# Kernel optimization log

Measured on AMD Instinct MI355X. Metric: run time of the kernel, lower is better.

The kernel has to match this reference:

```python
import jax, jax.numpy as jnp
import numpy as np

B, N, M, C1, C2 = 4, 8192, 2048, 128, 256
H1, H2 = 256, 128  # mlp = [C2+C1, 256, 128]
EPS_DIST = 1e-8
EPS_BN = 1e-5
K = 3


def setup_inputs() -> dict:
    key = jax.random.key(0)
    ks = jax.random.split(key, 6)
    return {
        "unknown": jax.random.normal(ks[0], (B, N, 3), dtype=jnp.float32),
        "known": jax.random.normal(ks[1], (B, M, 3), dtype=jnp.float32),
        "unknow_feats": jax.random.normal(ks[2], (B, C1, N), dtype=jnp.float32),
        "known_feats": jax.random.normal(ks[3], (B, C2, M), dtype=jnp.float32),
        "W1": jax.random.normal(ks[4], (H1, C1 + C2), dtype=jnp.float32) * 0.05,
        "g1": jnp.ones((H1,), jnp.float32),
        "b1": jnp.zeros((H1,), jnp.float32),
        "W2": jax.random.normal(ks[5], (H2, H1), dtype=jnp.float32) * 0.05,
        "g2": jnp.ones((H2,), jnp.float32),
        "b2": jnp.zeros((H2,), jnp.float32),
    }


def _bn_relu(x, g, b):
    # training-mode BatchNorm over (batch, spatial) axes for (B, C, N) tensor
    mean = jnp.mean(x, axis=(0, 2), keepdims=True)
    var = jnp.var(x, axis=(0, 2), keepdims=True)
    y = (x - mean) * jax.lax.rsqrt(var + EPS_BN) * g[None, :, None] + b[None, :, None]
    return jax.nn.relu(y)


def reference(unknown, known, unknow_feats, known_feats, W1, g1, b1, W2, g2, b2):
    # 3-NN: squared euclidean distances (B, N, M) via expansion (avoids B,N,M,3 temp)
    d2 = (
        jnp.sum(unknown * unknown, axis=-1)[:, :, None]
        + jnp.sum(known * known, axis=-1)[:, None, :]
        - 2.0 * jnp.einsum("bnc,bmc->bnm", unknown, known)
    )
    neg_d, idx = jax.lax.top_k(-d2, K)  # smallest-K squared dists
    dist = -neg_d  # (B, N, K), squared distances (pytorch3d knn_points convention)
    recip = 1.0 / (dist + EPS_DIST)
    weight = recip / jnp.sum(recip, axis=2, keepdims=True)  # (B, N, K)

    kf = jnp.swapaxes(known_feats, 1, 2)  # (B, M, C2)
    grouped = jax.vmap(lambda f, i: f[i])(kf, idx)  # (B, N, K, C2)
    interp = jnp.einsum("bnkc,bnk->bcn", grouped, weight)  # (B, C2, N)

    x = jnp.concatenate([interp, unknow_feats], axis=1)  # (B, C2+C1, N)
    x = _bn_relu(jnp.einsum("oc,bcn->bon", W1, x), g1, b1)
    x = _bn_relu(jnp.einsum("oc,bcn->bon", W2, x), g2, b2)
    return x  # (B, H2, N)
```

## Files before the change

kernel.cpp:

```cpp
#include <hip/hip_runtime.h>
#include <hip/hip_bf16.h>
#include <cstdint>
#include <cstddef>

typedef unsigned short u16;
typedef __attribute__((ext_vector_type(8))) short bf16x8;
typedef __attribute__((ext_vector_type(4))) float f32x4;

constexpr int Bn = 4;
constexpr int Nq = 8192;
constexpr int Mk = 2048;
constexpr int C1c = 128;
constexpr int C2c = 256;
constexpr int H1c = 256;
constexpr int H2c = 128;

__device__ __forceinline__ float bf2f(u16 u) {
    union { uint32_t i; float f; } v;
    v.i = (uint32_t)u << 16;
    return v.f;
}
__device__ __forceinline__ u16 f2bf(float f) {
    const uint32_t x = __float_as_uint(f);
    return (u16)((x + 0x7FFFu + ((x >> 16) & 1u)) >> 16);
}
__device__ __forceinline__ uint32_t cvtpk(float lo, float hi) {
    uint32_t r;
    asm("v_cvt_pk_bf16_f32 %0, %1, %2" : "=v"(r) : "v"(lo), "v"(hi));
    return r;
}

__global__ __launch_bounds__(256) void knn_prep_kernel(
    const float* __restrict__ W1, const float* __restrict__ W2,
    u16* __restrict__ W1b, u16* __restrict__ W2b,
    const float* __restrict__ KF, u16* __restrict__ Ptb,
    const float* __restrict__ unknown, const float* __restrict__ known,
    int* __restrict__ idx_out, float* __restrict__ w_out)
{
    __shared__ __align__(16) char smem[32768];
    const int bid = blockIdx.x;
    const int t = threadIdx.x;

    if (bid < 1024) {
        float4* kp = (float4*)smem;
        const int b = bid >> 8;
        const int n0 = (bid & 255) * 32;

        const float* kb = known + (size_t)b * Mk * 3;
        for (int i = t; i < Mk; i += 256) {
            const float x = kb[i * 3 + 0], y = kb[i * 3 + 1], z = kb[i * 3 + 2];
            kp[i] = make_float4(x, y, z, fmaf(x, x, fmaf(y, y, z * z)));
        }
        __syncthreads();

        const int q = n0 + (t >> 3);
        const int s = t & 7;
        const float* u = unknown + ((size_t)b * Nq + q) * 3;
        const float ux = u[0], uy = u[1], uz = u[2];
        const float nux = -2.0f * ux, nuy = -2.0f * uy, nuz = -2.0f * uz;
        const float uu = fmaf(ux, ux, fmaf(uy, uy, uz * uz));

        float d0 = 1e30f, d1 = 1e30f, d2 = 1e30f;
        int i0 = 0, i1 = 0, i2 = 0;

        auto ins = [&](float d, int i) {
            const bool c0 = d < d0, c1 = d < d1, c2 = d < d2;
            const float nd0 = fminf(d0, d);
            const float nd1 = __builtin_amdgcn_fmed3f(d0, d, d1);
            const float nd2 = __builtin_amdgcn_fmed3f(d1, d, d2);
            i2 = c1 ? i1 : (c2 ? i : i2);
            i1 = c0 ? i0 : (c1 ? i : i1);
            i0 = c0 ? i : i0;
            d0 = nd0; d1 = nd1; d2 = nd2;
        };

        #pragma unroll 8
        for (int it = 0; it < Mk / 8; ++it) {
            const int m = it * 8 + s;
            const float4 p = kp[m];
            const float d = fmaf(nux, p.x, fmaf(nuy, p.y, fmaf(nuz, p.z, p.w)));
            ins(d, m);
        }
        #pragma unroll
        for (int off = 1; off <= 4; off <<= 1) {
            const float e0 = __shfl_xor(d0, off), e1 = __shfl_xor(d1, off), e2 = __shfl_xor(d2, off);
            const int j0 = __shfl_xor(i0, off), j1 = __shfl_xor(i1, off), j2 = __shfl_xor(i2, off);
            ins(e0, j0);
            ins(e1, j1);
            ins(e2, j2);
        }
        if (s == 0) {
            const float f0 = d0 + uu, f1 = d1 + uu, f2 = d2 + uu;
            const float r0 = 1.0f / (f0 + 1e-8f);
            const float r1 = 1.0f / (f1 + 1e-8f);
            const float r2 = 1.0f / (f2 + 1e-8f);
            const float inv = 1.0f / (r0 + r1 + r2);
            const size_t base = ((size_t)b * Nq + q) * 3;
            idx_out[base + 0] = i0;
            idx_out[base + 1] = i1;
            idx_out[base + 2] = i2;
            w_out[base + 0] = r0 * inv;
            w_out[base + 1] = r1 * inv;
            w_out[base + 2] = r2 * inv;
        }
    } else if (bid < 1152) {
        const int cb = bid - 1024;
        const float* X = (cb < 96) ? W1 : W2;
        u16* Y = (cb < 96) ? W1b : W2b;
        const int i = ((cb < 96) ? cb : (cb - 96)) * 256 + t;
        const float4 v = *(const float4*)&X[(size_t)i * 4];
        ushort4 o;
        o.x = f2bf(v.x); o.y = f2bf(v.y); o.z = f2bf(v.z); o.w = f2bf(v.w);
        *(ushort4*)&Y[(size_t)i * 4] = o;
    } else {
        u16* As = (u16*)smem;
        u16* Bs = (u16*)(smem + 5120);
        const int f = bid - 1152;
        const int b = f >> 7;
        const int rem = f & 127;
        const int m0 = (rem >> 2) * 64;
        const int h0 = (rem & 3) * 64;
        const float* KFb = KF + (size_t)b * C2c * Mk;
        const int l = t & 63, wv = t >> 6;
        const int wr = wv >> 1, wc = wv & 1;

        f32x4 acc[2][2];
        const f32x4 z = {0.0f, 0.0f, 0.0f, 0.0f};
        acc[0][0] = z; acc[0][1] = z; acc[1][0] = z; acc[1][1] = z;

        const int cA = t >> 3;
        const int mcA = (t & 7) * 8;
        const int hB = t >> 2;
        const int khB = (t & 3) * 8;

        for (int kt = 0; kt < 8; ++kt) {
            const int kc = kt * 32;
            {
                const float* src = &KFb[(size_t)(kc + cA) * Mk + m0 + mcA];
                const float4 v0 = *(const float4*)&src[0];
                const float4 v1 = *(const float4*)&src[4];
                As[(mcA + 0) * 40 + cA] = f2bf(v0.x);
                As[(mcA + 1) * 40 + cA] = f2bf(v0.y);
                As[(mcA + 2) * 40 + cA] = f2bf(v0.z);
                As[(mcA + 3) * 40 + cA] = f2bf(v0.w);
                As[(mcA + 4) * 40 + cA] = f2bf(v1.x);
                As[(mcA + 5) * 40 + cA] = f2bf(v1.y);
                As[(mcA + 6) * 40 + cA] = f2bf(v1.z);
                As[(mcA + 7) * 40 + cA] = f2bf(v1.w);
            }
            {
                const float* src = &W1[(size_t)(h0 + hB) * 384 + kc + khB];
                const float4 v0 = *(const float4*)&src[0];
                const float4 v1 = *(const float4*)&src[4];
                u16 o[8] = {f2bf(v0.x), f2bf(v0.y), f2bf(v0.z), f2bf(v0.w),
                            f2bf(v1.x), f2bf(v1.y), f2bf(v1.z), f2bf(v1.w)};
                *(uint4*)&Bs[hB * 40 + khB] = *(const uint4*)o;
            }
            __syncthreads();
            bf16x8 af[2], bf[2];
            #pragma unroll
            for (int ff = 0; ff < 2; ++ff) {
                af[ff] = *(const bf16x8*)&As[(wr * 32 + ff * 16 + (l & 15)) * 40 + (l >> 4) * 8];
                bf[ff] = *(const bf16x8*)&Bs[(wc * 32 + ff * 16 + (l & 15)) * 40 + (l >> 4) * 8];
            }
            #pragma unroll
            for (int i = 0; i < 2; ++i)
                #pragma unroll
                for (int j = 0; j < 2; ++j)
                    acc[i][j] = __builtin_amdgcn_mfma_f32_16x16x32_bf16(af[i], bf[j], acc[i][j], 0, 0, 0);
            __syncthreads();
        }

        u16* Pb = Ptb + (size_t)b * Mk * 256;
        const int cb = l & 15, rg = (l >> 4) * 4;
        #pragma unroll
        for (int i = 0; i < 2; ++i) {
            #pragma unroll
            for (int r = 0; r < 4; ++r) {
                const int row = m0 + wr * 32 + i * 16 + rg + r;
                #pragma unroll
                for (int j = 0; j < 2; ++j)
                    Pb[(size_t)row * 256 + h0 + wc * 32 + j * 16 + cb] = f2bf(acc[i][j][r]);
            }
        }
    }
}

__global__ __launch_bounds__(256) void mfma_gemm2(
    const float* __restrict__ UF,
    const u16* __restrict__ Bt,
    u16* __restrict__ Cout,
    const u16* __restrict__ Ptb,
    const int* __restrict__ idx, const float* __restrict__ wgt,
    float* __restrict__ partS, float* __restrict__ partQ)
{
    __shared__ __align__(16) char smem[16384];
    __shared__ float redS[4][128], redQ[4][128];
    u16* As = (u16*)smem;
    u16* Bs = (u16*)(smem + 8192);
    float (*Ytmp)[128] = (float(*)[128])smem;

    const int b = blockIdx.z;
    const int m0 = blockIdx.x * 128, n0 = blockIdx.y * 128;
    const int t = threadIdx.x;
    const int l = t & 63, wv = t >> 6;
    const int wr = wv >> 1, wc = wv & 1;

    const float* UFb = UF + (size_t)b * C1c * Nq;
    const int p = t & 15;
    const int qg = t >> 4;
    const int rB0 = t >> 2, rB1v = (t + 256) >> 2;
    const int koB = (t & 3) * 8;

    f32x4 acc[4][4];
    const f32x4 z = {0.0f, 0.0f, 0.0f, 0.0f};
    #pragma unroll
    for (int i = 0; i < 4; ++i)
        #pragma unroll
        for (int j = 0; j < 4; ++j) acc[i][j] = z;

    float4 va0, va1, vb0, vb1;
    {
        const float* r0 = &UFb[(size_t)(2 * p) * Nq + m0 + qg * 8];
        const float* r1 = r0 + Nq;
        va0 = *(const float4*)&r0[0];
        va1 = *(const float4*)&r0[4];
        vb0 = *(const float4*)&r1[0];
        vb1 = *(const float4*)&r1[4];
    }
    uint4 b0 = *(const uint4*)&Bt[(size_t)(n0 + rB0) * 384 + koB];
    uint4 b1 = *(const uint4*)&Bt[(size_t)(n0 + rB1v) * 384 + koB];

    for (int kt = 0; kt < C1c / 32; ++kt) {
        {
            const float* la = (const float*)&va0;
            const float* lb = (const float*)&va1;
            const float* ha = (const float*)&vb0;
            const float* hb = (const float*)&vb1;
            #pragma unroll
            for (int i = 0; i < 8; ++i) {
                const int row = qg * 8 + i;
                const float lo = (i < 4) ? la[i] : lb[i - 4];
                const float hi = (i < 4) ? ha[i] : hb[i - 4];
                const int byte = row * 64 + ((((p >> 2) ^ (row & 3)) << 4)) + (p & 3) * 4;
                *(uint32_t*)((char*)As + byte) = cvtpk(lo, hi);
            }
        }
        *(uint4*)&Bs[(size_t)rB0 * 32 + koB] = b0;
        *(uint4*)&Bs[(size_t)rB1v * 32 + koB] = b1;
        __syncthreads();
        if (kt + 1 < C1c / 32) {
            const int k0 = (kt + 1) * 32;
            const float* r0 = &UFb[(size_t)(k0 + 2 * p) * Nq + m0 + qg * 8];
            const float* r1 = r0 + Nq;
            va0 = *(const float4*)&r0[0];
            va1 = *(const float4*)&r0[4];
            vb0 = *(const float4*)&r1[0];
            vb1 = *(const float4*)&r1[4];
            b0 = *(const uint4*)&Bt[(size_t)(n0 + rB0) * 384 + k0 + koB];
            b1 = *(const uint4*)&Bt[(size_t)(n0 + rB1v) * 384 + k0 + koB];
        }
        bf16x8 af[4], bf[4];
        #pragma unroll
        for (int f = 0; f < 4; ++f) {
            const int row = wr * 64 + f * 16 + (l & 15);
            af[f] = *(const bf16x8*)((char*)As + row * 64 + ((((l >> 4) ^ (l & 3)) << 4)));
            bf[f] = *(const bf16x8*)&Bs[(wc * 64 + f * 16 + (l & 15)) * 32 + (l >> 4) * 8];
        }
        #pragma unroll
        for (int i = 0; i < 4; ++i)
            #pragma unroll
            for (int j = 0; j < 4; ++j)
                acc[i][j] = __builtin_amdgcn_mfma_f32_16x16x32_bf16(af[i], bf[j], acc[i][j], 0, 0, 0);
        __syncthreads();
    }

    const int cb = l & 15;
    const int rg = (l >> 4) * 4;
    const int colblk = t & 15;
    const int rowblk = t >> 4;
    float s8[8] = {0, 0, 0, 0, 0, 0, 0, 0}, q8[8] = {0, 0, 0, 0, 0, 0, 0, 0};
    const u16* Pb = Ptb + (size_t)b * Mk * 256;

    for (int q = 0; q < 4; ++q) {
        __syncthreads();
        if (wr == (q >> 1)) {
            #pragma unroll
            for (int ii = 0; ii < 2; ++ii) {
                const int i = (q & 1) * 2 + ii;
                #pragma unroll
                for (int r = 0; r < 4; ++r) {
                    const int Rq = ii * 16 + rg + r;
                    #pragma unroll
                    for (int j = 0; j < 4; ++j)
                        Ytmp[Rq][wc * 64 + j * 16 + cb] = acc[i][j][r];
                }
            }
        }
        __syncthreads();
        #pragma unroll
        for (int rr = 0; rr < 2; ++rr) {
            const int Rq = rowblk * 2 + rr;
            const int R = m0 + q * 32 + Rq;
            const size_t ib = ((size_t)b * Nq + R) * 3;
            const int j0 = idx[ib], j1 = idx[ib + 1], j2 = idx[ib + 2];
            const float w0 = wgt[ib], w1 = wgt[ib + 1], w2 = wgt[ib + 2];
            const int c8 = colblk * 8;
            const int Cc0 = n0 + c8;
            const float* yrow = &Ytmp[Rq][c8];
            const float4 y0 = *(const float4*)&yrow[0];
            const float4 y1v = *(const float4*)&yrow[4];
            const uint4 p0 = *(const uint4*)&Pb[(size_t)j0 * 256 + Cc0];
            const uint4 p1 = *(const uint4*)&Pb[(size_t)j1 * 256 + Cc0];
            const uint4 p2 = *(const uint4*)&Pb[(size_t)j2 * 256 + Cc0];
            const u16* pp0 = (const u16*)&p0;
            const u16* pp1 = (const u16*)&p1;
            const u16* pp2 = (const u16*)&p2;
            const float* ya = (const float*)&y0;
            const float* yb = (const float*)&y1v;
            float v[8];
            #pragma unroll
            for (int c = 0; c < 8; ++c) {
                const float a = (c < 4) ? ya[c] : yb[c - 4];
                const float vv = a + w0 * bf2f(pp0[c]) + w1 * bf2f(pp1[c]) + w2 * bf2f(pp2[c]);
                v[c] = vv;
                s8[c] += vv;
                q8[c] += vv * vv;
            }
            uint4 o;
            uint32_t* po = (uint32_t*)&o;
            po[0] = cvtpk(v[0], v[1]);
            po[1] = cvtpk(v[2], v[3]);
            po[2] = cvtpk(v[4], v[5]);
            po[3] = cvtpk(v[6], v[7]);
            *(uint4*)&Cout[(size_t)b * Nq * 256 + (size_t)R * 256 + Cc0] = o;
        }
    }

    #pragma unroll
    for (int c = 0; c < 8; ++c) {
        s8[c] += __shfl_xor(s8[c], 16);
        s8[c] += __shfl_xor(s8[c], 32);
        q8[c] += __shfl_xor(q8[c], 16);
        q8[c] += __shfl_xor(q8[c], 32);
    }
    if (l < 16) {
        #pragma unroll
        for (int c = 0; c < 8; ++c) {
            redS[wv][l * 8 + c] = s8[c];
            redQ[wv][l * 8 + c] = q8[c];
        }
    }
    __syncthreads();
    if (t < 128) {
        const float S = redS[0][t] + redS[1][t] + redS[2][t] + redS[3][t];
        const float Q = redQ[0][t] + redQ[1][t] + redQ[2][t] + redQ[3][t];
        const int pblk = blockIdx.z * gridDim.x + blockIdx.x;
        partS[(size_t)pblk * 256 + blockIdx.y * 128 + t] = S;
        partQ[(size_t)pblk * 256 + blockIdx.y * 128 + t] = Q;
    }
}

__global__ __launch_bounds__(256) void bn1_finalize_mb(
    const float* __restrict__ pS, const float* __restrict__ pQ,
    const float* __restrict__ g, const float* __restrict__ beta,
    float* __restrict__ scale, float* __restrict__ bias)
{
    __shared__ float rs[256], rq[256];
    const int cc = threadIdx.x & 15;
    const int sl = threadIdx.x >> 4;
    const int ch = blockIdx.x * 16 + cc;
    float s = 0.0f, q = 0.0f;
    for (int i = sl; i < 256; i += 16) {
        s += pS[(size_t)i * 256 + ch];
        q += pQ[(size_t)i * 256 + ch];
    }
    rs[threadIdx.x] = s;
    rq[threadIdx.x] = q;
    __syncthreads();
    if (sl == 0) {
        for (int k = 1; k < 16; ++k) {
            s += rs[k * 16 + cc];
            q += rq[k * 16 + cc];
        }
        const float cnt = (float)(Bn * Nq);
        const float mean = s / cnt;
        const float var = q / cnt - mean * mean;
        const float rv = rsqrtf(var + 1e-5f);
        const float sc = g[ch] * rv;
        scale[ch] = sc;
        bias[ch] = beta[ch] - mean * sc;
    }
}

__device__ __forceinline__ uint4 bnx(uint4 x, const float* scs, const float* bis, int k) {
    const u16* p = (const u16*)&x;
    const float4 s0 = *(const float4*)&scs[k];
    const float4 s1 = *(const float4*)&scs[k + 4];
    const float4 b0 = *(const float4*)&bis[k];
    const float4 b1 = *(const float4*)&bis[k + 4];
    const float* sa = (const float*)&s0;
    const float* sb = (const float*)&s1;
    const float* ba = (const float*)&b0;
    const float* bb = (const float*)&b1;
    uint4 o;
    uint32_t* po = (uint32_t*)&o;
    #pragma unroll
    for (int w2 = 0; w2 < 2; ++w2) {
        const float a0 = fmaxf(0.0f, fmaf(bf2f(p[2 * w2 + 0]), sa[2 * w2 + 0], ba[2 * w2 + 0]));
        const float a1 = fmaxf(0.0f, fmaf(bf2f(p[2 * w2 + 1]), sa[2 * w2 + 1], ba[2 * w2 + 1]));
        po[w2] = cvtpk(a0, a1);
    }
    #pragma unroll
    for (int w2 = 0; w2 < 2; ++w2) {
        const float a0 = fmaxf(0.0f, fmaf(bf2f(p[4 + 2 * w2 + 0]), sb[2 * w2 + 0], bb[2 * w2 + 0]));
        const float a1 = fmaxf(0.0f, fmaf(bf2f(p[4 + 2 * w2 + 1]), sb[2 * w2 + 1], bb[2 * w2 + 1]));
        po[2 + w2] = cvtpk(a0, a1);
    }
    return o;
}

__global__ __launch_bounds__(256) void mfma_gemm3(
    const u16* __restrict__ W2b,
    const u16* __restrict__ Y,
    u16* __restrict__ y2b,
    const float* __restrict__ bn_s, const float* __restrict__ bn_b,
    float* __restrict__ partS, float* __restrict__ partQ)
{
    __shared__ u16 As[2048];
    __shared__ u16 Bs[4096];
    __shared__ float scs[256], bis[256];
    __shared__ float sS[2][64], sQ[2][64];

    const int b = blockIdx.z;
    const int m0 = blockIdx.x * 64;
    const int n0 = blockIdx.y * 128;
    const int t = threadIdx.x;
    const int l = t & 63, wv = t >> 6;
    const int wr = wv >> 1, wc = wv & 1;

    scs[t] = bn_s[t];
    bis[t] = bn_b[t];

    const u16* Yb = Y + (size_t)b * Nq * 256;
    const int rA = t >> 2;
    const int rB1 = (t + 256) >> 2;
    const int ko = (t & 3) * 8;

    f32x4 acc[2][4];
    const f32x4 z = {0.0f, 0.0f, 0.0f, 0.0f};
    #pragma unroll
    for (int i = 0; i < 2; ++i)
        #pragma unroll
        for (int j = 0; j < 4; ++j) acc[i][j] = z;

    uint4 a0 = *(const uint4*)&W2b[(size_t)(m0 + rA) * 256 + ko];
    uint4 b0 = *(const uint4*)&Yb[(size_t)(n0 + rA) * 256 + ko];
    uint4 b1 = *(const uint4*)&Yb[(size_t)(n0 + rB1) * 256 + ko];
    __syncthreads();

    for (int kt = 0; kt < 8; ++kt) {
        const int k = kt * 32 + ko;
        *(uint4*)&As[t * 8] = a0;
        *(uint4*)&Bs[t * 8] = bnx(b0, scs, bis, k);
        *(uint4*)&Bs[(t + 256) * 8] = bnx(b1, scs, bis, k);
        __syncthreads();
        if (kt + 1 < 8) {
            const int k0 = (kt + 1) * 32;
            a0 = *(const uint4*)&W2b[(size_t)(m0 + rA) * 256 + k0 + ko];
            b0 = *(const uint4*)&Yb[(size_t)(n0 + rA) * 256 + k0 + ko];
            b1 = *(const uint4*)&Yb[(size_t)(n0 + rB1) * 256 + k0 + ko];
        }
        bf16x8 af[2], bf[4];
        #pragma unroll
        for (int f = 0; f < 2; ++f)
            af[f] = *(const bf16x8*)&As[(wr * 32 + f * 16 + (l & 15)) * 32 + (l >> 4) * 8];
        #pragma unroll
        for (int f = 0; f < 4; ++f)
            bf[f] = *(const bf16x8*)&Bs[(wc * 64 + f * 16 + (l & 15)) * 32 + (l >> 4) * 8];
        #pragma unroll
        for (int i = 0; i < 2; ++i)
            #pragma unroll
            for (int j = 0; j < 4; ++j)
                acc[i][j] = __builtin_amdgcn_mfma_f32_16x16x32_bf16(af[i], bf[j], acc[i][j], 0, 0, 0);
        __syncthreads();
    }

    const int cb = l & 15;
    const int rg = (l >> 4) * 4;
    u16* ob = y2b + (size_t)b * H2c * Nq;
    #pragma unroll
    for (int i = 0; i < 2; ++i) {
        #pragma unroll
        for (int r = 0; r < 4; ++r) {
            const int Rl = wr * 32 + i * 16 + rg + r;
            #pragma unroll
            for (int j = 0; j < 4; ++j) {
                const int Cc = n0 + wc * 64 + j * 16 + cb;
                ob[(size_t)(m0 + Rl) * Nq + Cc] = f2bf(acc[i][j][r]);
            }
            float s = acc[i][0][r] + acc[i][1][r] + acc[i][2][r] + acc[i][3][r];
            float q = acc[i][0][r] * acc[i][0][r] + acc[i][1][r] * acc[i][1][r] +
                      acc[i][2][r] * acc[i][2][r] + acc[i][3][r] * acc[i][3][r];
            s += __shfl_xor(s, 1); s += __shfl_xor(s, 2);
            s += __shfl_xor(s, 4); s += __shfl_xor(s, 8);
            q += __shfl_xor(q, 1); q += __shfl_xor(q, 2);
            q += __shfl_xor(q, 4); q += __shfl_xor(q, 8);
            if ((l & 15) == 0) {
                sS[wc][Rl] = s;
                sQ[wc][Rl] = q;
            }
        }
    }
    __syncthreads();
    if (t < 64) {
        const float S = sS[0][t] + sS[1][t];
        const float Q = sQ[0][t] + sQ[1][t];
        const int p = blockIdx.z * gridDim.y + blockIdx.y;
        partS[(size_t)p * 128 + m0 + t] = S;
        partQ[(size_t)p * 128 + m0 + t] = Q;
    }
}

__global__ __launch_bounds__(256) void bn2_finalize_mb(
    const float* __restrict__ pS, const float* __restrict__ pQ,
    const float* __restrict__ g, const float* __restrict__ beta,
    float* __restrict__ scale, float* __restrict__ bias)
{
    __shared__ float rs[256], rq[256];
    const int cc = threadIdx.x & 15;
    const int sl = threadIdx.x >> 4;
    const int ch = blockIdx.x * 16 + cc;
    float s = 0.0f, q = 0.0f;
    for (int i = sl; i < 256; i += 16) {
        s += pS[(size_t)i * 128 + ch];
        q += pQ[(size_t)i * 128 + ch];
    }
    rs[threadIdx.x] = s;
    rq[threadIdx.x] = q;
    __syncthreads();
    if (sl == 0) {
        for (int k = 1; k < 16; ++k) {
            s += rs[k * 16 + cc];
            q += rq[k * 16 + cc];
        }
        const float cnt = (float)(Bn * Nq);
        const float mean = s / cnt;
        const float var = q / cnt - mean * mean;
        const float rv = rsqrtf(var + 1e-5f);
        const float sc = g[ch] * rv;
        scale[ch] = sc;
        bias[ch] = beta[ch] - mean * sc;
    }
}

__global__ __launch_bounds__(256) void bn2_apply_simple(
    const u16* __restrict__ y2b, float* __restrict__ out,
    const float* __restrict__ scale, const float* __restrict__ bias)
{
    const size_t base = (size_t)blockIdx.x * 2048;
    const int c = (int)((base / Nq) % H2c);
    const float sc = scale[c], bi = bias[c];
    const size_t i = base + threadIdx.x * 8;
    const uint4 v = *(const uint4*)&y2b[i];
    const u16* pv = (const u16*)&v;
    float4 o0, o1;
    o0.x = fmaxf(0.0f, fmaf(bf2f(pv[0]), sc, bi));
    o0.y = fmaxf(0.0f, fmaf(bf2f(pv[1]), sc, bi));
    o0.z = fmaxf(0.0f, fmaf(bf2f(pv[2]), sc, bi));
    o0.w = fmaxf(0.0f, fmaf(bf2f(pv[3]), sc, bi));
    o1.x = fmaxf(0.0f, fmaf(bf2f(pv[4]), sc, bi));
    o1.y = fmaxf(0.0f, fmaf(bf2f(pv[5]), sc, bi));
    o1.z = fmaxf(0.0f, fmaf(bf2f(pv[6]), sc, bi));
    o1.w = fmaxf(0.0f, fmaf(bf2f(pv[7]), sc, bi));
    *(float4*)&out[i] = o0;
    *(float4*)&out[i + 4] = o1;
}

extern "C" void kernel_launch(void* const* d_in, const int* in_sizes, int n_in,
                              void* d_out, int out_size, void* d_ws, size_t ws_size,
                              hipStream_t stream) {
    const float* unknown = (const float*)d_in[0];
    const float* known = (const float*)d_in[1];
    const float* unknow_feats = (const float*)d_in[2];
    const float* known_feats = (const float*)d_in[3];
    const float* W1 = (const float*)d_in[4];
    const float* g1 = (const float*)d_in[5];
    const float* b1 = (const float*)d_in[6];
    const float* W2 = (const float*)d_in[7];
    const float* g2 = (const float*)d_in[8];
    const float* b2 = (const float*)d_in[9];
    float* out = (float*)d_out;

    char* w = (char*)d_ws;
    u16* W1b = (u16*)w; w += (size_t)H1c * 384 * 2;
    u16* W2b = (u16*)w; w += (size_t)H2c * H1c * 2;
    u16* Ptb = (u16*)w; w += (size_t)Bn * Mk * H1c * 2;
    u16* y1b = (u16*)w; w += (size_t)Bn * Nq * H1c * 2;
    u16* y2b = (u16*)w; w += (size_t)Bn * H2c * Nq * 2;
    int* idx = (int*)w; w += (size_t)Bn * Nq * 3 * 4;
    float* wgt = (float*)w; w += (size_t)Bn * Nq * 3 * 4;
    float* pS1 = (float*)w; w += (size_t)256 * 256 * 4;
    float* pQ1 = (float*)w; w += (size_t)256 * 256 * 4;
    float* pS2 = (float*)w; w += (size_t)256 * 128 * 4;
    float* pQ2 = (float*)w; w += (size_t)256 * 128 * 4;
    float* scale1 = (float*)w; w += 1024;
    float* bias1 = (float*)w; w += 1024;
    float* scale2 = (float*)w; w += 1024;
    float* bias2 = (float*)w; w += 1024;

    knn_prep_kernel<<<1664, 256, 0, stream>>>(W1, W2, W1b, W2b,
                                              known_feats, Ptb,
                                              unknown, known, idx, wgt);

    mfma_gemm2<<<dim3(Nq / 128, H1c / 128, Bn), 256, 0, stream>>>(
        unknow_feats, W1b + C2c, y1b, Ptb, idx, wgt, pS1, pQ1);

    bn1_finalize_mb<<<16, 256, 0, stream>>>(pS1, pQ1, g1, b1, scale1, bias1);

    mfma_gemm3<<<dim3(2, Nq / 128, Bn), 256, 0, stream>>>(
        W2b, y1b, y2b, scale1, bias1, pS2, pQ2);

    bn2_finalize_mb<<<8, 256, 0, stream>>>(pS2, pQ2, g2, b2, scale2, bias2);

    bn2_apply_simple<<<(Bn * H2c * Nq) / 2048, 256, 0, stream>>>(y2b, out, scale2, bias2);
}
```

Baseline: 92.78 us.

## Restructure KNN to one query per lane with wave-uniform known loads

Each lane now owns one query, and each of the 4 waves scans a quarter of the known points. Known points are read straight from global memory with wave-uniform addresses (likely scalar loads), replacing the LDS staging pass. The top-3 insertion is skipped when no lane in the wave would improve its set, and the partial results from the 4 waves are merged through shared memory by the first wave. This halves the KNN block count and drops the 8-lane shuffle reduction, at the cost of recomputing |k|^2 per point, a divergent __any branch, and a serial cross-wave merge on one wave.

```diff
diff --git a/kernel.cpp b/kernel.cpp
--- a/kernel.cpp
+++ b/kernel.cpp
@@ -41,24 +41,16 @@
     const int bid = blockIdx.x;
     const int t = threadIdx.x;
 
-    if (bid < 1024) {
-        float4* kp = (float4*)smem;
-        const int b = bid >> 8;
-        const int n0 = (bid & 255) * 32;
-
-        const float* kb = known + (size_t)b * Mk * 3;
-        for (int i = t; i < Mk; i += 256) {
-            const float x = kb[i * 3 + 0], y = kb[i * 3 + 1], z = kb[i * 3 + 2];
-            kp[i] = make_float4(x, y, z, fmaf(x, x, fmaf(y, y, z * z)));
-        }
-        __syncthreads();
-
-        const int q = n0 + (t >> 3);
-        const int s = t & 7;
+    if (bid < 512) {
+        const int b = bid >> 7;
+        const int qbase = (bid & 127) * 64;
+        const int l = t & 63;
+        const int w = t >> 6;
+        const int q = qbase + l;
+
         const float* u = unknown + ((size_t)b * Nq + q) * 3;
         const float ux = u[0], uy = u[1], uz = u[2];
         const float nux = -2.0f * ux, nuy = -2.0f * uy, nuz = -2.0f * uz;
-        const float uu = fmaf(ux, ux, fmaf(uy, uy, uz * uz));
 
         float d0 = 1e30f, d1 = 1e30f, d2 = 1e30f;
         int i0 = 0, i1 = 0, i2 = 0;
@@ -74,37 +66,77 @@
             d0 = nd0; d1 = nd1; d2 = nd2;
         };
 
-        #pragma unroll 8
-        for (int it = 0; it < Mk / 8; ++it) {
-            const int m = it * 8 + s;
-            const float4 p = kp[m];
-            const float d = fmaf(nux, p.x, fmaf(nuy, p.y, fmaf(nuz, p.z, p.w)));
-            ins(d, m);
-        }
-        #pragma unroll
-        for (int off = 1; off <= 4; off <<= 1) {
-            const float e0 = __shfl_xor(d0, off), e1 = __shfl_xor(d1, off), e2 = __shfl_xor(d2, off);
-            const int j0 = __shfl_xor(i0, off), j1 = __shfl_xor(i1, off), j2 = __shfl_xor(i2, off);
-            ins(e0, j0);
-            ins(e1, j1);
-            ins(e2, j2);
-        }
-        if (s == 0) {
-            const float f0 = d0 + uu, f1 = d1 + uu, f2 = d2 + uu;
+        const float* kb = known + (size_t)b * Mk * 3;
+        const int mbase = w * 512;
+        #pragma unroll 4
+        for (int mi = 0; mi < 512; ++mi) {
+            const int m = mbase + mi;
+            const float sx = kb[m * 3 + 0];
+            const float sy = kb[m * 3 + 1];
+            const float sz = kb[m * 3 + 2];
+            const float kk = fmaf(sx, sx, fmaf(sy, sy, sz * sz));
+            const float d = fmaf(nux, sx, fmaf(nuy, sy, fmaf(nuz, sz, kk)));
+            if (__any(d < d2)) ins(d, m);
+        }
+
+        float* dW = (float*)smem;
+        int* iW = (int*)(smem + 4096);
+        const int base4 = (w * 64 + l) * 4;
+        dW[base4 + 0] = d0; dW[base4 + 1] = d1; dW[base4 + 2] = d2;
+        iW[base4 + 0] = i0; iW[base4 + 1] = i1; iW[base4 + 2] = i2;
+        __syncthreads();
+
+        if (t < 64) {
+            float D0 = dW[t * 4 + 0], D1 = dW[t * 4 + 1], D2 = dW[t * 4 + 2];
+            int I0 = iW[t * 4 + 0], I1 = iW[t * 4 + 1], I2 = iW[t * 4 + 2];
+            auto mins = [&](float d, int i) {
+                const bool c0 = d < D0, c1 = d < D1, c2 = d < D2;
+                const float nd0 = fminf(D0, d);
+                const float nd1 = __builtin_amdgcn_fmed3f(D0, d, D1);
+                const float nd2 = __builtin_amdgcn_fmed3f(D1, d, D2);
+                I2 = c1 ? I1 : (c2 ? i : I2);
+                I1 = c0 ? I0 : (c1 ? i : I1);
+                I0 = c0 ? i : I0;
+                D0 = nd0; D1 = nd1; D2 = nd2;
+            };
+            auto mins_hi = [&](float d, int i) {
+                const bool c1 = d < D1, c2 = d < D2;
+                const float nd1 = fminf(D1, d);
+                const float nd2 = __builtin_amdgcn_fmed3f(D1, d, D2);
+                I2 = c1 ? I1 : (c2 ? i : I2);
+                I1 = c1 ? i : I1;
+                D1 = nd1; D2 = nd2;
+            };
+            auto mins_top = [&](float d, int i) {
+                const bool c2 = d < D2;
+                D2 = fminf(D2, d);
+                I2 = c2 ? i : I2;
+            };
+            #pragma unroll
+            for (int ww = 1; ww < 4; ++ww) {
+                const int pb = (ww * 64 + t) * 4;
+                mins(dW[pb + 0], iW[pb + 0]);
+                mins_hi(dW[pb + 1], iW[pb + 1]);
+                mins_top(dW[pb + 2], iW[pb + 2]);
+            }
+            const float* uq = unknown + ((size_t)b * Nq + qbase + t) * 3;
+            const float qx = uq[0], qy = uq[1], qz = uq[2];
+            const float uu = fmaf(qx, qx, fmaf(qy, qy, qz * qz));
+            const float f0 = D0 + uu, f1 = D1 + uu, f2 = D2 + uu;
             const float r0 = 1.0f / (f0 + 1e-8f);
             const float r1 = 1.0f / (f1 + 1e-8f);
             const float r2 = 1.0f / (f2 + 1e-8f);
             const float inv = 1.0f / (r0 + r1 + r2);
-            const size_t base = ((size_t)b * Nq + q) * 3;
-            idx_out[base + 0] = i0;
-            idx_out[base + 1] = i1;
-            idx_out[base + 2] = i2;
-            w_out[base + 0] = r0 * inv;
-            w_out[base + 1] = r1 * inv;
-            w_out[base + 2] = r2 * inv;
-        }
-    } else if (bid < 1152) {
-        const int cb = bid - 1024;
+            const size_t obase = ((size_t)b * Nq + qbase + t) * 3;
+            idx_out[obase + 0] = I0;
+            idx_out[obase + 1] = I1;
+            idx_out[obase + 2] = I2;
+            w_out[obase + 0] = r0 * inv;
+            w_out[obase + 1] = r1 * inv;
+            w_out[obase + 2] = r2 * inv;
+        }
+    } else if (bid < 640) {
+        const int cb = bid - 512;
         const float* X = (cb < 96) ? W1 : W2;
         u16* Y = (cb < 96) ? W1b : W2b;
         const int i = ((cb < 96) ? cb : (cb - 96)) * 256 + t;
@@ -115,7 +147,7 @@
     } else {
         u16* As = (u16*)smem;
         u16* Bs = (u16*)(smem + 5120);
-        const int f = bid - 1152;
+        const int f = bid - 640;
         const int b = f >> 7;
         const int rem = f & 127;
         const int m0 = (rem >> 2) * 64;
@@ -609,7 +641,7 @@
     float* scale2 = (float*)w; w += 1024;
     float* bias2 = (float*)w; w += 1024;
 
-    knn_prep_kernel<<<1664, 256, 0, stream>>>(W1, W2, W1b, W2b,
+    knn_prep_kernel<<<1152, 256, 0, stream>>>(W1, W2, W1b, W2b,
                                               known_feats, Ptb,
                                               unknown, known, idx, wgt);
 
```

Measured after the change: 133.5 us. +43.9%, slower.
